# Kernel optimization log

Hardware: AMD Instinct MI355X
Metric: run time of the kernel (lower is better)

## Reference

```python
import jax, jax.numpy as jnp
import numpy as np

B, T, D = 16384, 3, 512   # batch, task_num, input_dim
G = T + 1                  # expert groups (idx 0 shared)
NE = 4                     # experts per group
H, E = 512, 256            # expert hidden, expert output dim (layers=[512,256])
GH = 256                   # gate hidden
TH, TO = 128, 64           # tower hidden / output dims


def setup_inputs() -> dict:
    key = jax.random.key(0)
    ks = jax.random.split(key, 14)
    s = 0.02
    return {
        "inputs": jax.random.normal(ks[0], (B, G, D), jnp.float32),
        # expert MLPs: [group, expert, ...]
        "expert_W1": jax.random.normal(ks[1], (G, NE, D, H), jnp.float32) * s,
        "expert_b1": jnp.zeros((G, NE, H), jnp.float32),
        "expert_W2": jax.random.normal(ks[2], (G, NE, H, E), jnp.float32) * s,
        "expert_b2": jnp.zeros((G, NE, E), jnp.float32),
        # per-task gates (softmax over G*NE experts)
        "gate_W1": jax.random.normal(ks[3], (T, D, GH), jnp.float32) * s,
        "gate_b1": jnp.zeros((T, GH), jnp.float32),
        "gate_W2": jax.random.normal(ks[4], (T, GH, G * NE), jnp.float32) * s,
        "gate_b2": jnp.zeros((T, G * NE), jnp.float32),
        # per-task towers (is_last=True)
        "tower_W1": jax.random.normal(ks[5], (T, E, TH), jnp.float32) * s,
        "tower_b1": jnp.zeros((T, TH), jnp.float32),
        "tower_W2": jax.random.normal(ks[6], (T, TH, TO), jnp.float32) * s,
        "tower_b2": jnp.zeros((T, TO), jnp.float32),
    }


def reference(inputs, expert_W1, expert_b1, expert_W2, expert_b2,
              gate_W1, gate_b1, gate_W2, gate_b2,
              tower_W1, tower_b1, tower_W2, tower_b2):
    b = inputs.shape[0]
    g, ne = expert_W1.shape[0], expert_W1.shape[1]
    t_num = gate_W1.shape[0]

    # All expert groups in one batched einsum: [B, G, NE, E]
    h1 = jax.nn.relu(jnp.einsum('bgd,gndh->bgnh', inputs, expert_W1) + expert_b1)
    emb = jnp.einsum('bgnh,gnhe->bgne', h1, expert_W2) + expert_b2

    # Task gates on (task input + shared input): softmax over G*NE experts
    gin = inputs[:, 1:, :] + inputs[:, :1, :]                      # [B, T, D]
    gh = jax.nn.relu(jnp.einsum('btd,tdh->bth', gin, gate_W1) + gate_b1)
    gw = jax.nn.softmax(jnp.einsum('bth,thk->btk', gh, gate_W2) + gate_b2, axis=-1)  # [B,T,G*NE]

    emb_sg = jax.lax.stop_gradient(emb)
    group_ids = jnp.arange(g)
    outs = []
    for t in range(t_num):
        # gradient flows only through shared group (0) and own group (t+1)
        keep = (group_ids == 0) | (group_ids == t + 1)              # [G]
        masked = jnp.where(keep[None, :, None, None], emb, emb_sg)  # [B,G,NE,E]
        agg = jnp.einsum('bk,bke->be', gw[:, t], masked.reshape(b, g * ne, -1))  # [B,E]
        th = jax.nn.relu(agg @ tower_W1[t] + tower_b1[t])
        outs.append(th @ tower_W2[t] + tower_b2[t])                 # [B,TO]
    return jnp.concatenate(outs, axis=1)                           # [B, T*TO]
```

## Files before the change

kernel.cpp:

```cpp
#include <hip/hip_runtime.h>
#include <math.h>

#define B_N  16384
#define T_N  3
#define D_N  512
#define G_N  4
#define NE_N 4
#define H_N  512
#define E_N  256
#define GH_N 256
#define K16  16
#define TH_N 128
#define TO_N 64

typedef __attribute__((ext_vector_type(8))) short short8;
typedef __attribute__((ext_vector_type(4))) float floatx4;

__device__ __forceinline__ unsigned short f2bf(float f) {
    union { float f; unsigned u; } v; v.f = f;
    unsigned r = (v.u + 0x7fffu + ((v.u >> 16) & 1u)) >> 16;
    return (unsigned short)r;
}
__device__ __forceinline__ float bf2f(unsigned short h) {
    union { unsigned u; float f; } v; v.u = ((unsigned)h) << 16;
    return v.f;
}
__device__ __forceinline__ unsigned pack2(float lo, float hi) {
    return ((unsigned)f2bf(hi) << 16) | (unsigned)f2bf(lo);
}

typedef const __attribute__((address_space(1))) void gvoid_t;
typedef __attribute__((address_space(3))) void lvoid_t;

#if __has_builtin(__builtin_amdgcn_global_load_lds)
#define HAVE_GLL 1
__device__ __forceinline__ void load_lds16(const void* g, void* l) {
    __builtin_amdgcn_global_load_lds((gvoid_t*)g, (lvoid_t*)l, 16, 0, 0);
}
#else
#define HAVE_GLL 0
#endif

__global__ __launch_bounds__(256) void convert_inputs(
    const float* __restrict__ x, unsigned short* __restrict__ xb,
    unsigned short* __restrict__ ginb)
{
    const long b = blockIdx.x;
    const int tid = threadIdx.x;
    const float* xr = x + b * (G_N * D_N);
    unsigned short* xo = xb + b * (G_N * D_N);
    unsigned short* go = ginb + b * (T_N * D_N);
    float2 v0 = *(const float2*)&xr[tid * 2];
    *(unsigned*)&xo[tid * 2] = pack2(v0.x, v0.y);
    #pragma unroll
    for (int g = 1; g < G_N; ++g) {
        float2 v = *(const float2*)&xr[g * D_N + tid * 2];
        *(unsigned*)&xo[g * D_N + tid * 2] = pack2(v.x, v.y);
        *(unsigned*)&go[(g - 1) * D_N + tid * 2] = pack2(v.x + v0.x, v.y + v0.y);
    }
}

__global__ __launch_bounds__(256) void prep_kernel(
    const float* __restrict__ eW1, const float* __restrict__ eW2,
    const float* __restrict__ gW1, const float* __restrict__ tW1,
    const float* __restrict__ tW2,
    unsigned short* __restrict__ W1t, unsigned short* __restrict__ W2t,
    unsigned short* __restrict__ G1t, unsigned short* __restrict__ TW1t,
    unsigned short* __restrict__ TW2t,
    const float* __restrict__ x, unsigned short* __restrict__ xb,
    unsigned short* __restrict__ ginb)
{
    const int bid = blockIdx.x;
    if (bid < 6648) {
        const float* in; unsigned short* out; int K, N, nx, local;
        if (bid < 4096)      { in = eW1; out = W1t;  K = 512; N = 512; nx = 16; local = bid; }
        else if (bid < 6144) { in = eW2; out = W2t;  K = 512; N = 256; nx = 8;  local = bid - 4096; }
        else if (bid < 6528) { in = gW1; out = G1t;  K = 512; N = 256; nx = 8;  local = bid - 6144; }
        else if (bid < 6624) { in = tW1; out = TW1t; K = 256; N = 128; nx = 4;  local = bid - 6528; }
        else                 { in = tW2; out = TW2t; K = 128; N = 64;  nx = 2;  local = bid - 6624; }
        const int ny = K / 32;
        const int xt = local % nx;
        const int yt = (local / nx) % ny;
        const int z  = local / (nx * ny);
        __shared__ float tile[32][33];
        const int tx = threadIdx.x & 31, ty = threadIdx.x >> 5;
        const long zo = (long)z * K * N;
        const int n0 = xt * 32, k0 = yt * 32;
        #pragma unroll
        for (int i = 0; i < 4; ++i)
            tile[ty + 8 * i][tx] = in[zo + (long)(k0 + ty + 8 * i) * N + n0 + tx];
        __syncthreads();
        #pragma unroll
        for (int i = 0; i < 4; ++i)
            out[zo + (long)(n0 + ty + 8 * i) * K + k0 + tx] = f2bf(tile[tx][ty + 8 * i]);
    } else {
        const long b = bid - 6648;
        const int tid = threadIdx.x;
        const float* xr = x + b * (G_N * D_N);
        unsigned short* xo = xb + b * (G_N * D_N);
        unsigned short* go = ginb + b * (T_N * D_N);
        float2 v0 = *(const float2*)&xr[tid * 2];
        *(unsigned*)&xo[tid * 2] = pack2(v0.x, v0.y);
        #pragma unroll
        for (int g = 1; g < G_N; ++g) {
            float2 v = *(const float2*)&xr[g * D_N + tid * 2];
            *(unsigned*)&xo[g * D_N + tid * 2] = pack2(v.x, v.y);
            *(unsigned*)&go[(g - 1) * D_N + tid * 2] = pack2(v.x + v0.x, v.y + v0.y);
        }
    }
}

__global__ __launch_bounds__(256, 2) void moe_fused(
    const unsigned short* __restrict__ xb,
    const unsigned short* __restrict__ W1t,
    const float* __restrict__ eb1,
    const unsigned short* __restrict__ W2t,
    const float* __restrict__ eb2,
    unsigned short* __restrict__ embb,
    const unsigned short* __restrict__ ginb,
    const unsigned short* __restrict__ G1t,
    const float* __restrict__ gb1,
    const float* __restrict__ gW2,
    const float* __restrict__ gb2,
    float* __restrict__ gw,
    int panels)
{
    __shared__ __align__(16) unsigned short sm[33792];
    const int tid = threadIdx.x;
    const int bid = blockIdx.x;
    const int nGate = 3 * panels;

    const int lane16 = tid & 15;
    const int quad = (tid & 63) >> 4;
    const int wave = tid >> 6;
    const int srow = tid >> 2;
    const int scolsw = (((tid & 3) ^ ((tid >> 3) & 3)) * 8);
    const int cw8 = ((quad ^ ((lane16 >> 1) & 3)) * 8);
    const int wm = (wave >> 1) * 64;
    const int wn = (wave & 1) * 64;

    if (bid < nGate) {
        unsigned short* As  = sm;
        unsigned short* Bs  = sm + 4096;
        unsigned short* w2s = sm + 8192;
        unsigned short* ghs = sm + 12416;

        const int t = bid / panels;
        const long b0 = (long)(bid % panels) * 128;
        const unsigned short* Ab = ginb + b0 * 1536 + (long)t * 512;

        {
            const float* W2p = gW2 + (long)t * (GH_N * K16) + (long)tid * K16;
            float4 w0 = *(const float4*)(W2p);
            float4 w1 = *(const float4*)(W2p + 4);
            float4 w2 = *(const float4*)(W2p + 8);
            float4 w3 = *(const float4*)(W2p + 12);
            w2s[ 0 * 264 + tid] = f2bf(w0.x); w2s[ 1 * 264 + tid] = f2bf(w0.y);
            w2s[ 2 * 264 + tid] = f2bf(w0.z); w2s[ 3 * 264 + tid] = f2bf(w0.w);
            w2s[ 4 * 264 + tid] = f2bf(w1.x); w2s[ 5 * 264 + tid] = f2bf(w1.y);
            w2s[ 6 * 264 + tid] = f2bf(w1.z); w2s[ 7 * 264 + tid] = f2bf(w1.w);
            w2s[ 8 * 264 + tid] = f2bf(w2.x); w2s[ 9 * 264 + tid] = f2bf(w2.y);
            w2s[10 * 264 + tid] = f2bf(w2.z); w2s[11 * 264 + tid] = f2bf(w2.w);
            w2s[12 * 264 + tid] = f2bf(w3.x); w2s[13 * 264 + tid] = f2bf(w3.y);
            w2s[14 * 264 + tid] = f2bf(w3.z); w2s[15 * 264 + tid] = f2bf(w3.w);
        }

        floatx4 ag[2] = {};
        #pragma unroll
        for (int ncc = 0; ncc < 2; ++ncc) {
            const unsigned short* Bb = G1t + (long)t * 131072 + (long)(ncc * 128) * 512;
            floatx4 acc[4][4] = {};
            for (int k0 = 0; k0 < 512; k0 += 32) {
#if HAVE_GLL
                load_lds16(Ab + (long)srow * 1536 + k0 + scolsw, &As[tid * 8]);
                load_lds16(Ab + (long)(srow + 64) * 1536 + k0 + scolsw, &As[2048 + tid * 8]);
                load_lds16(Bb + (long)srow * 512 + k0 + scolsw, &Bs[tid * 8]);
                load_lds16(Bb + (long)(srow + 64) * 512 + k0 + scolsw, &Bs[2048 + tid * 8]);
#else
                *(uint4*)&As[tid * 8] = *(const uint4*)(Ab + (long)srow * 1536 + k0 + scolsw);
                *(uint4*)&As[2048 + tid * 8] = *(const uint4*)(Ab + (long)(srow + 64) * 1536 + k0 + scolsw);
                *(uint4*)&Bs[tid * 8] = *(const uint4*)(Bb + (long)srow * 512 + k0 + scolsw);
                *(uint4*)&Bs[2048 + tid * 8] = *(const uint4*)(Bb + (long)(srow + 64) * 512 + k0 + scolsw);
#endif
                __syncthreads();
                short8 a[4], b[4];
                #pragma unroll
                for (int mi = 0; mi < 4; ++mi)
                    a[mi] = *(const short8*)&As[(wm + mi * 16 + lane16) * 32 + cw8];
                #pragma unroll
                for (int ni = 0; ni < 4; ++ni)
                    b[ni] = *(const short8*)&Bs[(wn + ni * 16 + lane16) * 32 + cw8];
                #pragma unroll
                for (int mi = 0; mi < 4; ++mi)
                    #pragma unroll
                    for (int ni = 0; ni < 4; ++ni)
                        acc[mi][ni] = __builtin_amdgcn_mfma_f32_16x16x32_bf16(
                            a[mi], b[ni], acc[mi][ni], 0, 0, 0);
                __syncthreads();
            }
            #pragma unroll
            for (int mi = 0; mi < 4; ++mi) {
                #pragma unroll
                for (int ni = 0; ni < 4; ++ni) {
                    const int col = wn + ni * 16 + lane16;
                    const float bv = gb1[t * GH_N + ncc * 128 + col];
                    #pragma unroll
                    for (int r = 0; r < 4; ++r) {
                        const int row = wm + mi * 16 + quad * 4 + r;
                        ghs[row * 136 + col] = f2bf(fmaxf(acc[mi][ni][r] + bv, 0.0f));
                    }
                }
            }
            __syncthreads();
            #pragma unroll
            for (int kk = 0; kk < 4; ++kk) {
                short8 bfr = *(const short8*)&w2s[lane16 * 264 + ncc * 128 + kk * 32 + quad * 8];
                #pragma unroll
                for (int mi = 0; mi < 2; ++mi) {
                    const int row = wave * 32 + mi * 16 + lane16;
                    short8 afr = *(const short8*)&ghs[row * 136 + kk * 32 + quad * 8];
                    ag[mi] = __builtin_amdgcn_mfma_f32_16x16x32_bf16(afr, bfr, ag[mi], 0, 0, 0);
                }
            }
        }

        const float bb2 = gb2[t * K16 + lane16];
        #pragma unroll
        for (int mi = 0; mi < 2; ++mi) {
            float v[4];
            #pragma unroll
            for (int r = 0; r < 4; ++r) v[r] = ag[mi][r] + bb2;
            #pragma unroll
            for (int r = 0; r < 4; ++r) {
                float mv = v[r];
                #pragma unroll
                for (int d = 1; d < 16; d <<= 1) mv = fmaxf(mv, __shfl_xor(mv, d));
                float e = expf(v[r] - mv);
                float s = e;
                #pragma unroll
                for (int d = 1; d < 16; d <<= 1) s += __shfl_xor(s, d);
                const int row = wave * 32 + mi * 16 + quad * 4 + r;
                gw[(b0 + row) * (T_N * K16) + (long)t * K16 + lane16] = e / s;
            }
        }
        return;
    }

    unsigned short* As  = sm;
    unsigned short* Bs  = sm + 8192;
    unsigned short* h1s = sm + 16384;

    const unsigned ebid = bid - nGate;
    const int e = ((ebid & 7) << 1) | ((ebid >> 3) & 1);
    const long m0 = (long)(ebid >> 4) * 128;
    const int g = e >> 2;

    const unsigned short* Ab  = xb + m0 * 2048 + g * 512;
    const unsigned short* W1b = W1t + (long)e * (512 * 512);
    const unsigned short* W2b = W2t + (long)e * (256 * 512);

    const int wn2 = (wave & 1) * 128;

    floatx4 acc2[4][8] = {};

    for (int nc = 0; nc < 4; ++nc) {
        const unsigned short* Bb = W1b + ((long)nc << 16);
        floatx4 acc[4][4] = {};
        for (int k0 = 0; k0 < 512; k0 += 64) {
            #pragma unroll
            for (int h = 0; h < 2; ++h) {
                const int kh = k0 + h * 32;
#if HAVE_GLL
                load_lds16(Ab + (long)srow * 2048 + kh + scolsw, &As[h * 4096 + tid * 8]);
                load_lds16(Ab + (long)(srow + 64) * 2048 + kh + scolsw, &As[h * 4096 + 2048 + tid * 8]);
                load_lds16(Bb + (long)srow * 512 + kh + scolsw, &Bs[h * 4096 + tid * 8]);
                load_lds16(Bb + (long)(srow + 64) * 512 + kh + scolsw, &Bs[h * 4096 + 2048 + tid * 8]);
#else
                *(uint4*)&As[h * 4096 + tid * 8] = *(const uint4*)(Ab + (long)srow * 2048 + kh + scolsw);
                *(uint4*)&As[h * 4096 + 2048 + tid * 8] = *(const uint4*)(Ab + (long)(srow + 64) * 2048 + kh + scolsw);
                *(uint4*)&Bs[h * 4096 + tid * 8] = *(const uint4*)(Bb + (long)srow * 512 + kh + scolsw);
                *(uint4*)&Bs[h * 4096 + 2048 + tid * 8] = *(const uint4*)(Bb + (long)(srow + 64) * 512 + kh + scolsw);
#endif
            }
            __syncthreads();
            #pragma unroll
            for (int h = 0; h < 2; ++h) {
                short8 b[4];
                #pragma unroll
                for (int ni = 0; ni < 4; ++ni)
                    b[ni] = *(const short8*)&Bs[h * 4096 + (wn + ni * 16 + lane16) * 32 + cw8];
                #pragma unroll
                for (int mi = 0; mi < 4; ++mi) {
                    short8 a = *(const short8*)&As[h * 4096 + (wm + mi * 16 + lane16) * 32 + cw8];
                    #pragma unroll
                    for (int ni = 0; ni < 4; ++ni)
                        acc[mi][ni] = __builtin_amdgcn_mfma_f32_16x16x32_bf16(
                            a, b[ni], acc[mi][ni], 0, 0, 0);
                }
            }
            __syncthreads();
        }
        #pragma unroll
        for (int mi = 0; mi < 4; ++mi) {
            #pragma unroll
            for (int ni = 0; ni < 4; ++ni) {
                const int col = wn + ni * 16 + lane16;
                const float bv = eb1[e * 512 + nc * 128 + col];
                #pragma unroll
                for (int r = 0; r < 4; ++r) {
                    const int row = wm + mi * 16 + quad * 4 + r;
                    h1s[row * 136 + col] = f2bf(fmaxf(acc[mi][ni][r] + bv, 0.0f));
                }
            }
        }
        __syncthreads();
        #pragma unroll
        for (int ks = 0; ks < 128; ks += 32) {
            #pragma unroll
            for (int i = 0; i < 4; ++i) {
#if HAVE_GLL
                load_lds16(W2b + (long)(srow + 64 * i) * 512 + nc * 128 + ks + scolsw,
                           &As[i * 2048 + tid * 8]);
#else
                *(uint4*)&As[i * 2048 + tid * 8] =
                    *(const uint4*)(W2b + (long)(srow + 64 * i) * 512 + nc * 128 + ks + scolsw);
#endif
            }
            __syncthreads();
            #pragma unroll
            for (int nh = 0; nh < 2; ++nh) {
                short8 b2[4];
                #pragma unroll
                for (int nj = 0; nj < 4; ++nj)
                    b2[nj] = *(const short8*)&As[(wn2 + nh * 64 + nj * 16 + lane16) * 32 + cw8];
                #pragma unroll
                for (int mi = 0; mi < 4; ++mi) {
                    short8 a2 = *(const short8*)&h1s[(wm + mi * 16 + lane16) * 136 + ks + quad * 8];
                    #pragma unroll
                    for (int nj = 0; nj < 4; ++nj)
                        acc2[mi][nh * 4 + nj] = __builtin_amdgcn_mfma_f32_16x16x32_bf16(
                            a2, b2[nj], acc2[mi][nh * 4 + nj], 0, 0, 0);
                }
            }
            __syncthreads();
        }
    }

    unsigned short* Cb = embb + m0 * 4096 + (long)e * 256;
    #pragma unroll
    for (int mi = 0; mi < 4; ++mi) {
        #pragma unroll
        for (int j = 0; j < 8; ++j) {
            const int col = wn2 + (j >> 2) * 64 + (j & 3) * 16 + lane16;
            const float bv = eb2[e * 256 + col];
            #pragma unroll
            for (int r = 0; r < 4; ++r) {
                const int row = wm + mi * 16 + quad * 4 + r;
                Cb[(long)row * 4096 + col] = f2bf(acc2[mi][j][r] + bv);
            }
        }
    }
}

__global__ __launch_bounds__(256) void agg_tower(
    const unsigned short* __restrict__ embb,
    const float* __restrict__ gw,
    const unsigned short* __restrict__ w1t,
    const float* __restrict__ tb1,
    const unsigned short* __restrict__ w2t,
    const float* __restrict__ tb2,
    float* __restrict__ out)
{
    __shared__ __align__(16) unsigned short sm[37888];
    const int tid = threadIdx.x;
    const int t = blockIdx.y;
    const long b0 = (long)blockIdx.x * 128;
    const int lane16 = tid & 15;
    const int quad = (tid & 63) >> 4;
    const int wave = tid >> 6;
    const int wm = (wave >> 1) * 64;
    const int wn = (wave & 1) * 64;
    const int srow = tid >> 2;
    const int scolsw = (((tid & 3) ^ ((tid >> 3) & 3)) * 8);
    const int cw8 = ((quad ^ ((lane16 >> 1) & 3)) * 8);

    float* gws = (float*)(sm + 33792);
    {
        const int r = tid >> 1, j0 = (tid & 1) * 8;
        const float* gp = gw + (b0 + r) * (T_N * K16) + (long)t * K16 + j0;
        *(float4*)&gws[r * 16 + j0]     = *(const float4*)gp;
        *(float4*)&gws[r * 16 + j0 + 4] = *(const float4*)(gp + 4);
    }
    __syncthreads();

    {
        const int gidx = tid & 31;
        const int r0 = tid >> 5;
        const int col8 = gidx * 8;
        #pragma unroll
        for (int i = 0; i < 16; ++i) {
            const int row = r0 + 8 * i;
            const unsigned short* er = embb + (b0 + row) * 4096 + col8;
            float a8[8] = {};
            #pragma unroll
            for (int k = 0; k < 16; ++k) {
                short8 v = *(const short8*)(er + (long)k * 256);
                const float w = gws[row * 16 + k];
                #pragma unroll
                for (int j = 0; j < 8; ++j) a8[j] += w * bf2f((unsigned short)v[j]);
            }
            unsigned rr[4] = {pack2(a8[0], a8[1]), pack2(a8[2], a8[3]),
                              pack2(a8[4], a8[5]), pack2(a8[6], a8[7])};
            *(uint4*)&sm[row * 264 + ((gidx ^ (row & 7)) * 8)] = *(uint4*)rr;
        }
    }
    __syncthreads();

    unsigned short* Bs = sm + 33792;
    const unsigned short* Bb = w1t + (long)t * (TH_N * E_N);
    floatx4 acc[4][4] = {};
    for (int k0 = 0; k0 < 256; k0 += 32) {
#if HAVE_GLL
        load_lds16(Bb + (long)srow * 256 + k0 + scolsw, &Bs[tid * 8]);
        load_lds16(Bb + (long)(srow + 64) * 256 + k0 + scolsw, &Bs[2048 + tid * 8]);
#else
        *(uint4*)&Bs[tid * 8] = *(const uint4*)(Bb + (long)srow * 256 + k0 + scolsw);
        *(uint4*)&Bs[2048 + tid * 8] = *(const uint4*)(Bb + (long)(srow + 64) * 256 + k0 + scolsw);
#endif
        __syncthreads();
        short8 a[4], b[4];
        #pragma unroll
        for (int mi = 0; mi < 4; ++mi) {
            const int row = wm + mi * 16 + lane16;
            const int gg = ((k0 >> 3) + quad) ^ (row & 7);
            a[mi] = *(const short8*)&sm[row * 264 + gg * 8];
        }
        #pragma unroll
        for (int ni = 0; ni < 4; ++ni)
            b[ni] = *(const short8*)&Bs[(wn + ni * 16 + lane16) * 32 + cw8];
        #pragma unroll
        for (int mi = 0; mi < 4; ++mi)
            #pragma unroll
            for (int ni = 0; ni < 4; ++ni)
                acc[mi][ni] = __builtin_amdgcn_mfma_f32_16x16x32_bf16(
                    a[mi], b[ni], acc[mi][ni], 0, 0, 0);
        __syncthreads();
    }

    unsigned short* th  = sm;
    unsigned short* w2s = sm + 17408;
    #pragma unroll
    for (int mi = 0; mi < 4; ++mi) {
        #pragma unroll
        for (int ni = 0; ni < 4; ++ni) {
            const int col = wn + ni * 16 + lane16;
            const float bv = tb1[t * TH_N + col];
            #pragma unroll
            for (int r = 0; r < 4; ++r) {
                const int row = wm + mi * 16 + quad * 4 + r;
                th[row * 136 + col] = f2bf(fmaxf(acc[mi][ni][r] + bv, 0.0f));
            }
        }
    }
    #pragma unroll
    for (int i = 0; i < 4; ++i) {
        const int seg = i * 256 + tid;
        const int row = seg >> 4, cb = (seg & 15) * 8;
        *(uint4*)&w2s[row * 136 + cb] =
            *(const uint4*)&w2t[(long)t * (TO_N * TH_N) + (long)row * 128 + cb];
    }
    __syncthreads();

    floatx4 acc2[2][4] = {};
    #pragma unroll
    for (int kk = 0; kk < 4; ++kk) {
        short8 a2[2], b2[4];
        #pragma unroll
        for (int mi = 0; mi < 2; ++mi)
            a2[mi] = *(const short8*)&th[(wave * 32 + mi * 16 + lane16) * 136 + kk * 32 + quad * 8];
        #pragma unroll
        for (int ni = 0; ni < 4; ++ni)
            b2[ni] = *(const short8*)&w2s[(ni * 16 + lane16) * 136 + kk * 32 + quad * 8];
        #pragma unroll
        for (int mi = 0; mi < 2; ++mi)
            #pragma unroll
            for (int ni = 0; ni < 4; ++ni)
                acc2[mi][ni] = __builtin_amdgcn_mfma_f32_16x16x32_bf16(
                    a2[mi], b2[ni], acc2[mi][ni], 0, 0, 0);
    }
    #pragma unroll
    for (int mi = 0; mi < 2; ++mi) {
        #pragma unroll
        for (int ni = 0; ni < 4; ++ni) {
            const int col = ni * 16 + lane16;
            const float bv = tb2[t * TO_N + col];
            #pragma unroll
            for (int r = 0; r < 4; ++r) {
                const int row = wave * 32 + mi * 16 + quad * 4 + r;
                out[(b0 + row) * (T_N * TO_N) + t * TO_N + col] = acc2[mi][ni][r] + bv;
            }
        }
    }
}

extern "C" void kernel_launch(void* const* d_in, const int* in_sizes, int n_in,
                              void* d_out, int out_size, void* d_ws, size_t ws_size,
                              hipStream_t stream)
{
    const float* x   = (const float*)d_in[0];
    const float* eW1 = (const float*)d_in[1];
    const float* eb1 = (const float*)d_in[2];
    const float* eW2 = (const float*)d_in[3];
    const float* eb2 = (const float*)d_in[4];
    const float* gW1 = (const float*)d_in[5];
    const float* gb1 = (const float*)d_in[6];
    const float* gW2 = (const float*)d_in[7];
    const float* gb2 = (const float*)d_in[8];
    const float* tW1 = (const float*)d_in[9];
    const float* tb1 = (const float*)d_in[10];
    const float* tW2 = (const float*)d_in[11];
    const float* tb2 = (const float*)d_in[12];
    float* out = (float*)d_out;

    char* ws = (char*)d_ws;
    unsigned short* W1t  = (unsigned short*)(ws + 0);
    unsigned short* W2t  = (unsigned short*)(ws + 8388608);
    unsigned short* G1t  = (unsigned short*)(ws + 12582912);
    unsigned short* TW1t = (unsigned short*)(ws + 13369344);
    unsigned short* TW2t = (unsigned short*)(ws + 13565952);
    const size_t WFIX = 13615104;

    long BCo = 0;
    for (long co = 16384; co >= 128; co >>= 1)
        if (WFIX + (size_t)co * 18624 <= ws_size) { BCo = co; break; }
    if (BCo == 0) return;

    char* p = ws + WFIX;
    unsigned short* xb   = (unsigned short*)p; p += BCo * 4096;
    unsigned short* ginb = (unsigned short*)p; p += BCo * 3072;
    unsigned short* embb = (unsigned short*)p; p += BCo * 8192;
    p += BCo * 1536;
    float*          gw   = (float*)p;          p += BCo * 192;

    const long n_o = B_N / BCo;
    const int panels = (int)(BCo / 128);

    const long nconv = (n_o == 1) ? BCo : 0;
    prep_kernel<<<dim3((unsigned)(6648 + nconv)), 256, 0, stream>>>(
        eW1, eW2, gW1, tW1, tW2, W1t, W2t, G1t, TW1t, TW2t, x, xb, ginb);

    for (long c = 0; c < n_o; ++c) {
        const float* xc = x + c * BCo * (G_N * D_N);
        float* outc = out + c * BCo * (T_N * TO_N);

        if (n_o > 1)
            convert_inputs<<<BCo, 256, 0, stream>>>(xc, xb, ginb);
        moe_fused<<<dim3((unsigned)(panels * 19)), 256, 0, stream>>>(
            xb, W1t, eb1, W2t, eb2, embb,
            ginb, G1t, gb1, gW2, gb2, gw, panels);
        agg_tower<<<dim3(panels, 3), 256, 0, stream>>>(
            embb, gw, TW1t, tb1, TW2t, tb2, outc);
    }
}
```

Measured before the change: 565.4 us.

## Split fused MoE kernel into 256x256 triple-buffered expert GEMMs with h1 staging

Replaces the combined gate+expert kernel, which kept the hidden activation in LDS, with a separate gate kernel and two batched 256x256-tile GEMM launches per chunk. The first GEMM computes relu(x@W1) for all 16 experts and writes bf16 h1 to workspace; the second multiplies h1 by W2 into the embedding buffer. Each GEMM uses a 512-thread block, three-stage LDS buffering with explicit vmcnt waits, and raised wave priority around the MFMAs. The aim is higher MFMA utilization and operand reuse from larger tiles. The cost is an extra global round trip for h1, plus workspace sizing logic that may split the batch into sub-chunks.

```diff
diff --git a/kernel.cpp b/kernel.cpp
--- a/kernel.cpp
+++ b/kernel.cpp
@@ -110,194 +110,195 @@
     }
 }
 
-__global__ __launch_bounds__(256, 2) void moe_fused(
-    const unsigned short* __restrict__ xb,
-    const unsigned short* __restrict__ W1t,
-    const float* __restrict__ eb1,
-    const unsigned short* __restrict__ W2t,
-    const float* __restrict__ eb2,
-    unsigned short* __restrict__ embb,
+template<int RELU>
+__global__ __launch_bounds__(512) void gemm256(
+    const unsigned short* __restrict__ A, int lda, long a_zoff, int a_zshift,
+    const unsigned short* __restrict__ Bt, long bt_zoff,
+    const float* __restrict__ bias, int bias_zoff,
+    unsigned short* __restrict__ C, int ldc, long c_zoff, int K)
+{
+    __shared__ __align__(16) unsigned short sm[49152];
+    const int tid = threadIdx.x;
+    const int z = blockIdx.z;
+    const long m0 = (long)blockIdx.x * 256;
+    const long n0 = (long)blockIdx.y * 256;
+    const unsigned short* Az = A + (long)(z >> a_zshift) * a_zoff + m0 * lda;
+    const unsigned short* Bz = Bt + (long)z * bt_zoff + n0 * K;
+
+    const int lane16 = tid & 15;
+    const int quad = (tid & 63) >> 4;
+    const int wave = tid >> 6;
+    const int wr = wave >> 2;
+    const int wc = wave & 3;
+    const int cwq = ((quad ^ ((lane16 >> 1) & 3)) * 8);
+    const int sr = tid >> 2;
+    const int sc = (((tid & 3) ^ ((tid >> 3) & 3)) * 8);
+
+    const unsigned short* Ag0 = Az + (long)sr * lda + sc;
+    const unsigned short* Ag1 = Az + (long)(sr + 128) * lda + sc;
+    const unsigned short* Bg0 = Bz + (long)sr * K + sc;
+    const unsigned short* Bg1 = Bz + (long)(sr + 128) * K + sc;
+
+    const int ntiles = K >> 5;
+
+    #pragma unroll
+    for (int t0 = 0; t0 < 2; ++t0) {
+        const int kk = t0 * 32;
+        unsigned short* d = &sm[t0 * 16384];
+#if HAVE_GLL
+        load_lds16(Ag0 + kk, &d[tid * 8]);
+        load_lds16(Ag1 + kk, &d[(512 + tid) * 8]);
+        load_lds16(Bg0 + kk, &d[8192 + tid * 8]);
+        load_lds16(Bg1 + kk, &d[8192 + (512 + tid) * 8]);
+#else
+        *(uint4*)&d[tid * 8] = *(const uint4*)(Ag0 + kk);
+        *(uint4*)&d[(512 + tid) * 8] = *(const uint4*)(Ag1 + kk);
+        *(uint4*)&d[8192 + tid * 8] = *(const uint4*)(Bg0 + kk);
+        *(uint4*)&d[8192 + (512 + tid) * 8] = *(const uint4*)(Bg1 + kk);
+#endif
+    }
+    asm volatile("s_waitcnt vmcnt(4)" ::: "memory");
+    __builtin_amdgcn_s_barrier();
+
+    floatx4 acc[8][4] = {};
+    int cur = 0;
+    for (int t = 0; t < ntiles; ++t) {
+        if (t + 2 < ntiles) {
+            int nb = cur + 2; if (nb >= 3) nb -= 3;
+            const int kk = (t + 2) * 32;
+            unsigned short* d = &sm[nb * 16384];
+#if HAVE_GLL
+            load_lds16(Ag0 + kk, &d[tid * 8]);
+            load_lds16(Ag1 + kk, &d[(512 + tid) * 8]);
+            load_lds16(Bg0 + kk, &d[8192 + tid * 8]);
+            load_lds16(Bg1 + kk, &d[8192 + (512 + tid) * 8]);
+#else
+            *(uint4*)&d[tid * 8] = *(const uint4*)(Ag0 + kk);
+            *(uint4*)&d[(512 + tid) * 8] = *(const uint4*)(Ag1 + kk);
+            *(uint4*)&d[8192 + tid * 8] = *(const uint4*)(Bg0 + kk);
+            *(uint4*)&d[8192 + (512 + tid) * 8] = *(const uint4*)(Bg1 + kk);
+#endif
+        }
+        const unsigned short* Abl = &sm[cur * 16384 + (wr * 128 + lane16) * 32 + cwq];
+        const unsigned short* Bbl = &sm[cur * 16384 + 8192 + (wc * 64 + lane16) * 32 + cwq];
+        short8 b[4];
+        #pragma unroll
+        for (int ni = 0; ni < 4; ++ni) b[ni] = *(const short8*)&Bbl[ni * 512];
+        short8 a[8];
+        #pragma unroll
+        for (int mi = 0; mi < 8; ++mi) a[mi] = *(const short8*)&Abl[mi * 512];
+        __builtin_amdgcn_s_setprio(1);
+        #pragma unroll
+        for (int mi = 0; mi < 8; ++mi)
+            #pragma unroll
+            for (int ni = 0; ni < 4; ++ni)
+                acc[mi][ni] = __builtin_amdgcn_mfma_f32_16x16x32_bf16(
+                    a[mi], b[ni], acc[mi][ni], 0, 0, 0);
+        __builtin_amdgcn_s_setprio(0);
+        if (t < ntiles - 2) {
+            asm volatile("s_waitcnt vmcnt(4)" ::: "memory");
+            __builtin_amdgcn_s_barrier();
+        } else if (t == ntiles - 2) {
+            asm volatile("s_waitcnt vmcnt(0)" ::: "memory");
+            __builtin_amdgcn_s_barrier();
+        }
+        ++cur; if (cur == 3) cur = 0;
+    }
+
+    unsigned short* Cb = C + (long)z * c_zoff + m0 * ldc + n0;
+    const float* bz = bias + (long)z * bias_zoff + n0;
+    #pragma unroll
+    for (int mi = 0; mi < 8; ++mi) {
+        #pragma unroll
+        for (int ni = 0; ni < 4; ++ni) {
+            const int col = wc * 64 + ni * 16 + lane16;
+            const float bv = bz[col];
+            #pragma unroll
+            for (int r = 0; r < 4; ++r) {
+                const int row = wr * 128 + mi * 16 + quad * 4 + r;
+                float v = acc[mi][ni][r] + bv;
+                if (RELU) v = fmaxf(v, 0.0f);
+                Cb[(long)row * ldc + col] = f2bf(v);
+            }
+        }
+    }
+}
+
+__global__ __launch_bounds__(256) void gate_fused(
     const unsigned short* __restrict__ ginb,
     const unsigned short* __restrict__ G1t,
     const float* __restrict__ gb1,
     const float* __restrict__ gW2,
     const float* __restrict__ gb2,
-    float* __restrict__ gw,
-    int panels)
+    float* __restrict__ gw)
 {
-    __shared__ __align__(16) unsigned short sm[33792];
+    __shared__ __align__(16) unsigned short sm[40960];
+    unsigned short* As  = sm;
+    unsigned short* Bs  = sm + 4096;
+    unsigned short* w2s = sm + 8192;
+    unsigned short* ghs = sm + 12416;
+
     const int tid = threadIdx.x;
-    const int bid = blockIdx.x;
-    const int nGate = 3 * panels;
+    const int t = blockIdx.y;
+    const long b0 = (long)blockIdx.x * 128;
+    const unsigned short* Ab = ginb + b0 * 1536 + (long)t * 512;
 
     const int lane16 = tid & 15;
     const int quad = (tid & 63) >> 4;
     const int wave = tid >> 6;
-    const int srow = tid >> 2;
-    const int scolsw = (((tid & 3) ^ ((tid >> 3) & 3)) * 8);
-    const int cw8 = ((quad ^ ((lane16 >> 1) & 3)) * 8);
     const int wm = (wave >> 1) * 64;
     const int wn = (wave & 1) * 64;
-
-    if (bid < nGate) {
-        unsigned short* As  = sm;
-        unsigned short* Bs  = sm + 4096;
-        unsigned short* w2s = sm + 8192;
-        unsigned short* ghs = sm + 12416;
-
-        const int t = bid / panels;
-        const long b0 = (long)(bid % panels) * 128;
-        const unsigned short* Ab = ginb + b0 * 1536 + (long)t * 512;
-
-        {
-            const float* W2p = gW2 + (long)t * (GH_N * K16) + (long)tid * K16;
-            float4 w0 = *(const float4*)(W2p);
-            float4 w1 = *(const float4*)(W2p + 4);
-            float4 w2 = *(const float4*)(W2p + 8);
-            float4 w3 = *(const float4*)(W2p + 12);
-            w2s[ 0 * 264 + tid] = f2bf(w0.x); w2s[ 1 * 264 + tid] = f2bf(w0.y);
-            w2s[ 2 * 264 + tid] = f2bf(w0.z); w2s[ 3 * 264 + tid] = f2bf(w0.w);
-            w2s[ 4 * 264 + tid] = f2bf(w1.x); w2s[ 5 * 264 + tid] = f2bf(w1.y);
-            w2s[ 6 * 264 + tid] = f2bf(w1.z); w2s[ 7 * 264 + tid] = f2bf(w1.w);
-            w2s[ 8 * 264 + tid] = f2bf(w2.x); w2s[ 9 * 264 + tid] = f2bf(w2.y);
-            w2s[10 * 264 + tid] = f2bf(w2.z); w2s[11 * 264 + tid] = f2bf(w2.w);
-            w2s[12 * 264 + tid] = f2bf(w3.x); w2s[13 * 264 + tid] = f2bf(w3.y);
-            w2s[14 * 264 + tid] = f2bf(w3.z); w2s[15 * 264 + tid] = f2bf(w3.w);
-        }
-
-        floatx4 ag[2] = {};
-        #pragma unroll
-        for (int ncc = 0; ncc < 2; ++ncc) {
-            const unsigned short* Bb = G1t + (long)t * 131072 + (long)(ncc * 128) * 512;
-            floatx4 acc[4][4] = {};
-            for (int k0 = 0; k0 < 512; k0 += 32) {
+    const int srow = tid >> 2;
+    const int scol = (((tid & 3) ^ ((tid >> 3) & 3)) * 8);
+    const int cw8 = ((quad ^ ((lane16 >> 1) & 3)) * 8);
+
+    {
+        const float* W2p = gW2 + (long)t * (GH_N * K16) + (long)tid * K16;
+        float4 w0 = *(const float4*)(W2p);
+        float4 w1 = *(const float4*)(W2p + 4);
+        float4 w2 = *(const float4*)(W2p + 8);
+        float4 w3 = *(const float4*)(W2p + 12);
+        w2s[ 0 * 264 + tid] = f2bf(w0.x); w2s[ 1 * 264 + tid] = f2bf(w0.y);
+        w2s[ 2 * 264 + tid] = f2bf(w0.z); w2s[ 3 * 264 + tid] = f2bf(w0.w);
+        w2s[ 4 * 264 + tid] = f2bf(w1.x); w2s[ 5 * 264 + tid] = f2bf(w1.y);
+        w2s[ 6 * 264 + tid] = f2bf(w1.z); w2s[ 7 * 264 + tid] = f2bf(w1.w);
+        w2s[ 8 * 264 + tid] = f2bf(w2.x); w2s[ 9 * 264 + tid] = f2bf(w2.y);
+        w2s[10 * 264 + tid] = f2bf(w2.z); w2s[11 * 264 + tid] = f2bf(w2.w);
+        w2s[12 * 264 + tid] = f2bf(w3.x); w2s[13 * 264 + tid] = f2bf(w3.y);
+        w2s[14 * 264 + tid] = f2bf(w3.z); w2s[15 * 264 + tid] = f2bf(w3.w);
+    }
+
+    floatx4 ag[2] = {};
+    #pragma unroll
+    for (int ncc = 0; ncc < 2; ++ncc) {
+        const unsigned short* Bb = G1t + (long)t * 131072 + (long)(ncc * 128) * 512;
+        floatx4 acc[4][4] = {};
+        for (int k0 = 0; k0 < 512; k0 += 32) {
 #if HAVE_GLL
-                load_lds16(Ab + (long)srow * 1536 + k0 + scolsw, &As[tid * 8]);
-                load_lds16(Ab + (long)(srow + 64) * 1536 + k0 + scolsw, &As[2048 + tid * 8]);
-                load_lds16(Bb + (long)srow * 512 + k0 + scolsw, &Bs[tid * 8]);
-                load_lds16(Bb + (long)(srow + 64) * 512 + k0 + scolsw, &Bs[2048 + tid * 8]);
+            load_lds16(Ab + (long)srow * 1536 + k0 + scol, &As[tid * 8]);
+            load_lds16(Ab + (long)(srow + 64) * 1536 + k0 + scol, &As[2048 + tid * 8]);
+            load_lds16(Bb + (long)srow * 512 + k0 + scol, &Bs[tid * 8]);
+            load_lds16(Bb + (long)(srow + 64) * 512 + k0 + scol, &Bs[2048 + tid * 8]);
 #else
-                *(uint4*)&As[tid * 8] = *(const uint4*)(Ab + (long)srow * 1536 + k0 + scolsw);
-                *(uint4*)&As[2048 + tid * 8] = *(const uint4*)(Ab + (long)(srow + 64) * 1536 + k0 + scolsw);
-                *(uint4*)&Bs[tid * 8] = *(const uint4*)(Bb + (long)srow * 512 + k0 + scolsw);
-                *(uint4*)&Bs[2048 + tid * 8] = *(const uint4*)(Bb + (long)(srow + 64) * 512 + k0 + scolsw);
+            *(uint4*)&As[tid * 8] = *(const uint4*)(Ab + (long)srow * 1536 + k0 + scol);
+            *(uint4*)&As[2048 + tid * 8] = *(const uint4*)(Ab + (long)(srow + 64) * 1536 + k0 + scol);
+            *(uint4*)&Bs[tid * 8] = *(const uint4*)(Bb + (long)srow * 512 + k0 + scol);
+            *(uint4*)&Bs[2048 + tid * 8] = *(const uint4*)(Bb + (long)(srow + 64) * 512 + k0 + scol);
 #endif
-                __syncthreads();
-                short8 a[4], b[4];
-                #pragma unroll
-                for (int mi = 0; mi < 4; ++mi)
-                    a[mi] = *(const short8*)&As[(wm + mi * 16 + lane16) * 32 + cw8];
+            __syncthreads();
+            short8 a[4], b[4];
+            #pragma unroll
+            for (int mi = 0; mi < 4; ++mi)
+                a[mi] = *(const short8*)&As[(wm + mi * 16 + lane16) * 32 + cw8];
+            #pragma unroll
+            for (int ni = 0; ni < 4; ++ni)
+                b[ni] = *(const short8*)&Bs[(wn + ni * 16 + lane16) * 32 + cw8];
+            #pragma unroll
+            for (int mi = 0; mi < 4; ++mi)
                 #pragma unroll
                 for (int ni = 0; ni < 4; ++ni)
-                    b[ni] = *(const short8*)&Bs[(wn + ni * 16 + lane16) * 32 + cw8];
-                #pragma unroll
-                for (int mi = 0; mi < 4; ++mi)
-                    #pragma unroll
-                    for (int ni = 0; ni < 4; ++ni)
-                        acc[mi][ni] = __builtin_amdgcn_mfma_f32_16x16x32_bf16(
-                            a[mi], b[ni], acc[mi][ni], 0, 0, 0);
-                __syncthreads();
-            }
-            #pragma unroll
-            for (int mi = 0; mi < 4; ++mi) {
-                #pragma unroll
-                for (int ni = 0; ni < 4; ++ni) {
-                    const int col = wn + ni * 16 + lane16;
-                    const float bv = gb1[t * GH_N + ncc * 128 + col];
-                    #pragma unroll
-                    for (int r = 0; r < 4; ++r) {
-                        const int row = wm + mi * 16 + quad * 4 + r;
-                        ghs[row * 136 + col] = f2bf(fmaxf(acc[mi][ni][r] + bv, 0.0f));
-                    }
-                }
-            }
-            __syncthreads();
-            #pragma unroll
-            for (int kk = 0; kk < 4; ++kk) {
-                short8 bfr = *(const short8*)&w2s[lane16 * 264 + ncc * 128 + kk * 32 + quad * 8];
-                #pragma unroll
-                for (int mi = 0; mi < 2; ++mi) {
-                    const int row = wave * 32 + mi * 16 + lane16;
-                    short8 afr = *(const short8*)&ghs[row * 136 + kk * 32 + quad * 8];
-                    ag[mi] = __builtin_amdgcn_mfma_f32_16x16x32_bf16(afr, bfr, ag[mi], 0, 0, 0);
-                }
-            }
-        }
-
-        const float bb2 = gb2[t * K16 + lane16];
-        #pragma unroll
-        for (int mi = 0; mi < 2; ++mi) {
-            float v[4];
-            #pragma unroll
-            for (int r = 0; r < 4; ++r) v[r] = ag[mi][r] + bb2;
-            #pragma unroll
-            for (int r = 0; r < 4; ++r) {
-                float mv = v[r];
-                #pragma unroll
-                for (int d = 1; d < 16; d <<= 1) mv = fmaxf(mv, __shfl_xor(mv, d));
-                float e = expf(v[r] - mv);
-                float s = e;
-                #pragma unroll
-                for (int d = 1; d < 16; d <<= 1) s += __shfl_xor(s, d);
-                const int row = wave * 32 + mi * 16 + quad * 4 + r;
-                gw[(b0 + row) * (T_N * K16) + (long)t * K16 + lane16] = e / s;
-            }
-        }
-        return;
-    }
-
-    unsigned short* As  = sm;
-    unsigned short* Bs  = sm + 8192;
-    unsigned short* h1s = sm + 16384;
-
-    const unsigned ebid = bid - nGate;
-    const int e = ((ebid & 7) << 1) | ((ebid >> 3) & 1);
-    const long m0 = (long)(ebid >> 4) * 128;
-    const int g = e >> 2;
-
-    const unsigned short* Ab  = xb + m0 * 2048 + g * 512;
-    const unsigned short* W1b = W1t + (long)e * (512 * 512);
-    const unsigned short* W2b = W2t + (long)e * (256 * 512);
-
-    const int wn2 = (wave & 1) * 128;
-
-    floatx4 acc2[4][8] = {};
-
-    for (int nc = 0; nc < 4; ++nc) {
-        const unsigned short* Bb = W1b + ((long)nc << 16);
-        floatx4 acc[4][4] = {};
-        for (int k0 = 0; k0 < 512; k0 += 64) {
-            #pragma unroll
-            for (int h = 0; h < 2; ++h) {
-                const int kh = k0 + h * 32;
-#if HAVE_GLL
-                load_lds16(Ab + (long)srow * 2048 + kh + scolsw, &As[h * 4096 + tid * 8]);
-                load_lds16(Ab + (long)(srow + 64) * 2048 + kh + scolsw, &As[h * 4096 + 2048 + tid * 8]);
-                load_lds16(Bb + (long)srow * 512 + kh + scolsw, &Bs[h * 4096 + tid * 8]);
-                load_lds16(Bb + (long)(srow + 64) * 512 + kh + scolsw, &Bs[h * 4096 + 2048 + tid * 8]);
-#else
-                *(uint4*)&As[h * 4096 + tid * 8] = *(const uint4*)(Ab + (long)srow * 2048 + kh + scolsw);
-                *(uint4*)&As[h * 4096 + 2048 + tid * 8] = *(const uint4*)(Ab + (long)(srow + 64) * 2048 + kh + scolsw);
-                *(uint4*)&Bs[h * 4096 + tid * 8] = *(const uint4*)(Bb + (long)srow * 512 + kh + scolsw);
-                *(uint4*)&Bs[h * 4096 + 2048 + tid * 8] = *(const uint4*)(Bb + (long)(srow + 64) * 512 + kh + scolsw);
-#endif
-            }
-            __syncthreads();
-            #pragma unroll
-            for (int h = 0; h < 2; ++h) {
-                short8 b[4];
-                #pragma unroll
-                for (int ni = 0; ni < 4; ++ni)
-                    b[ni] = *(const short8*)&Bs[h * 4096 + (wn + ni * 16 + lane16) * 32 + cw8];
-                #pragma unroll
-                for (int mi = 0; mi < 4; ++mi) {
-                    short8 a = *(const short8*)&As[h * 4096 + (wm + mi * 16 + lane16) * 32 + cw8];
-                    #pragma unroll
-                    for (int ni = 0; ni < 4; ++ni)
-                        acc[mi][ni] = __builtin_amdgcn_mfma_f32_16x16x32_bf16(
-                            a, b[ni], acc[mi][ni], 0, 0, 0);
-                }
-            }
+                    acc[mi][ni] = __builtin_amdgcn_mfma_f32_16x16x32_bf16(
+                        a[mi], b[ni], acc[mi][ni], 0, 0, 0);
             __syncthreads();
         }
         #pragma unroll
@@ -305,59 +306,44 @@
             #pragma unroll
             for (int ni = 0; ni < 4; ++ni) {
                 const int col = wn + ni * 16 + lane16;
-                const float bv = eb1[e * 512 + nc * 128 + col];
+                const float bv = gb1[t * GH_N + ncc * 128 + col];
                 #pragma unroll
                 for (int r = 0; r < 4; ++r) {
                     const int row = wm + mi * 16 + quad * 4 + r;
-                    h1s[row * 136 + col] = f2bf(fmaxf(acc[mi][ni][r] + bv, 0.0f));
+                    ghs[row * 136 + col] = f2bf(fmaxf(acc[mi][ni][r] + bv, 0.0f));
                 }
             }
         }
         __syncthreads();
         #pragma unroll
-        for (int ks = 0; ks < 128; ks += 32) {
-            #pragma unroll
-            for (int i = 0; i < 4; ++i) {
-#if HAVE_GLL
-                load_lds16(W2b + (long)(srow + 64 * i) * 512 + nc * 128 + ks + scolsw,
-                           &As[i * 2048 + tid * 8]);
-#else
-                *(uint4*)&As[i * 2048 + tid * 8] =
-                    *(const uint4*)(W2b + (long)(srow + 64 * i) * 512 + nc * 128 + ks + scolsw);
-#endif
+        for (int kk = 0; kk < 4; ++kk) {
+            short8 bfr = *(const short8*)&w2s[lane16 * 264 + ncc * 128 + kk * 32 + quad * 8];
+            #pragma unroll
+            for (int mi = 0; mi < 2; ++mi) {
+                const int row = wave * 32 + mi * 16 + lane16;
+                short8 afr = *(const short8*)&ghs[row * 136 + kk * 32 + quad * 8];
+                ag[mi] = __builtin_amdgcn_mfma_f32_16x16x32_bf16(afr, bfr, ag[mi], 0, 0, 0);
             }
-            __syncthreads();
-            #pragma unroll
-            for (int nh = 0; nh < 2; ++nh) {
-                short8 b2[4];
-                #pragma unroll
-                for (int nj = 0; nj < 4; ++nj)
-                    b2[nj] = *(const short8*)&As[(wn2 + nh * 64 + nj * 16 + lane16) * 32 + cw8];
-                #pragma unroll
-                for (int mi = 0; mi < 4; ++mi) {
-                    short8 a2 = *(const short8*)&h1s[(wm + mi * 16 + lane16) * 136 + ks + quad * 8];
-                    #pragma unroll
-                    for (int nj = 0; nj < 4; ++nj)
-                        acc2[mi][nh * 4 + nj] = __builtin_amdgcn_mfma_f32_16x16x32_bf16(
-                            a2, b2[nj], acc2[mi][nh * 4 + nj], 0, 0, 0);
-                }
-            }
-            __syncthreads();
-        }
-    }
-
-    unsigned short* Cb = embb + m0 * 4096 + (long)e * 256;
-    #pragma unroll
-    for (int mi = 0; mi < 4; ++mi) {
-        #pragma unroll
-        for (int j = 0; j < 8; ++j) {
-            const int col = wn2 + (j >> 2) * 64 + (j & 3) * 16 + lane16;
-            const float bv = eb2[e * 256 + col];
-            #pragma unroll
-            for (int r = 0; r < 4; ++r) {
-                const int row = wm + mi * 16 + quad * 4 + r;
-                Cb[(long)row * 4096 + col] = f2bf(acc2[mi][j][r] + bv);
-            }
+        }
+    }
+
+    const float bb2 = gb2[t * K16 + lane16];
+    #pragma unroll
+    for (int mi = 0; mi < 2; ++mi) {
+        float v[4];
+        #pragma unroll
+        for (int r = 0; r < 4; ++r) v[r] = ag[mi][r] + bb2;
+        #pragma unroll
+        for (int r = 0; r < 4; ++r) {
+            float mv = v[r];
+            #pragma unroll
+            for (int d = 1; d < 16; d <<= 1) mv = fmaxf(mv, __shfl_xor(mv, d));
+            float e = expf(v[r] - mv);
+            float s = e;
+            #pragma unroll
+            for (int d = 1; d < 16; d <<= 1) s += __shfl_xor(s, d);
+            const int row = wave * 32 + mi * 16 + quad * 4 + r;
+            gw[(b0 + row) * (T_N * K16) + (long)t * K16 + lane16] = e / s;
         }
     }
 }
@@ -530,20 +516,25 @@
     unsigned short* TW2t = (unsigned short*)(ws + 13565952);
     const size_t WFIX = 13615104;
 
-    long BCo = 0;
-    for (long co = 16384; co >= 128; co >>= 1)
-        if (WFIX + (size_t)co * 18624 <= ws_size) { BCo = co; break; }
+    long BCo = 0, BCh = 0;
+    for (long co = 16384; co >= 256; co >>= 1) {
+        size_t base = WFIX + (size_t)co * 15552;
+        if (base + (size_t)256 * 16384 > ws_size) continue;
+        long ch = 0;
+        for (long c2 = co; c2 >= 256; c2 >>= 1)
+            if (base + (size_t)c2 * 16384 <= ws_size) { ch = c2; break; }
+        if (ch) { BCo = co; BCh = ch; break; }
+    }
     if (BCo == 0) return;
 
     char* p = ws + WFIX;
     unsigned short* xb   = (unsigned short*)p; p += BCo * 4096;
     unsigned short* ginb = (unsigned short*)p; p += BCo * 3072;
     unsigned short* embb = (unsigned short*)p; p += BCo * 8192;
-    p += BCo * 1536;
     float*          gw   = (float*)p;          p += BCo * 192;
+    unsigned short* h1   = (unsigned short*)p;
 
     const long n_o = B_N / BCo;
-    const int panels = (int)(BCo / 128);
 
     const long nconv = (n_o == 1) ? BCo : 0;
     prep_kernel<<<dim3((unsigned)(6648 + nconv)), 256, 0, stream>>>(
@@ -555,10 +546,19 @@
 
         if (n_o > 1)
             convert_inputs<<<BCo, 256, 0, stream>>>(xc, xb, ginb);
-        moe_fused<<<dim3((unsigned)(panels * 19)), 256, 0, stream>>>(
-            xb, W1t, eb1, W2t, eb2, embb,
-            ginb, G1t, gb1, gW2, gb2, gw, panels);
-        agg_tower<<<dim3(panels, 3), 256, 0, stream>>>(
+        gate_fused<<<dim3(BCo / 128, 3), 256, 0, stream>>>(
+            ginb, G1t, gb1, gW2, gb2, gw);
+        for (long d = 0; d < BCo / BCh; ++d) {
+            gemm256<1><<<dim3(BCh / 256, 2, 16), 512, 0, stream>>>(
+                xb + d * BCh * 2048, 2048, 512, 2,
+                W1t, 262144, eb1, 512,
+                h1, 8192, 512, 512);
+            gemm256<0><<<dim3(BCh / 256, 1, 16), 512, 0, stream>>>(
+                h1, 8192, 512, 0,
+                W2t, 131072, eb2, 256,
+                embb + d * BCh * 4096, 4096, 256, 512);
+        }
+        agg_tower<<<dim3(BCo / 128, 3), 256, 0, stream>>>(
             embb, gw, TW1t, tb1, TW2t, tb2, outc);
     }
 }
```

New measurement: 647.9 us. 14.6% more time.
